# Optimization experiments

Measured on AMD Instinct MI355X. Metric: run time of the kernel, lower is better.

Reference implementation:

```python
import jax, jax.numpy as jnp
import numpy as np

NUM_HEADS = 8
HEAD_DIM = 32
ATTN_DIM = NUM_HEADS * HEAD_DIM  # 256
WINDOW_SIZES = (7, 5)
DILATIONS = (1, 2)
SCALE_FACTORS = (2, 4)


def conv1x1(x, W, b):
    # x: [B, C, H, W], W: [O, C], b: [O]
    return jnp.einsum('bchw,oc->bohw', x, W) + b[None, :, None, None]


def gather_neighbors(x, window, dilation):
    """Zero-padded dilated neighborhood gather.
    x: [B, C, h, w] -> neighbors [B, C, K, h, w], valid mask [K, h, w] (K = window**2)."""
    B, C, h, w = x.shape
    pad = dilation * (window // 2)
    xp = jnp.pad(x, ((0, 0), (0, 0), (pad, pad), (pad, pad)))
    mp = jnp.pad(jnp.ones((h, w), dtype=bool), ((pad, pad), (pad, pad)))
    neigh, masks = [], []
    for i in range(window):
        for j in range(window):
            dy, dx = dilation * i, dilation * j
            neigh.append(xp[:, :, dy:dy + h, dx:dx + w])
            masks.append(mp[dy:dy + h, dx:dx + w])
    return jnp.stack(neigh, axis=2), jnp.stack(masks, axis=0)


def align_to_query_grid(t, Hq, Wq, sf):
    """Repeat coarse-lattice candidates onto the fine query grid via anchor indexing."""
    y = jnp.minimum(jnp.arange(Hq) // sf, t.shape[-2] - 1)
    x = jnp.minimum(jnp.arange(Wq) // sf, t.shape[-1] - 1)
    return jnp.take(jnp.take(t, y, axis=-2), x, axis=-1)


def _forward(query, mems, Wq, bq, Wks, bks, Wvs, bvs, Wfuse, bfuse):
    B, _, Hq, Wq_ = query.shape
    q = conv1x1(query, Wq, bq)                                  # [B, attn, Hq, Wq]
    qh = q.reshape(B, NUM_HEADS, HEAD_DIM, Hq, Wq_)             # [B, n, d, H, W]
    scale = HEAD_DIM ** -0.5
    outs = []
    for s, mem in enumerate(mems):
        k = conv1x1(mem, Wks[s], bks[s])                        # [B, attn, hm, wm]
        v = conv1x1(mem, Wvs[s], bvs[s])
        kn, mask = gather_neighbors(k, WINDOW_SIZES[s], DILATIONS[s])  # [B, attn, K, hm, wm]
        vn, _ = gather_neighbors(v, WINDOW_SIZES[s], DILATIONS[s])
        K = kn.shape[2]
        hm, wm = kn.shape[-2:]
        kn = kn.reshape(B, NUM_HEADS, HEAD_DIM, K, hm, wm).transpose(0, 1, 3, 2, 4, 5)  # [B,n,K,d,hm,wm]
        vn = vn.reshape(B, NUM_HEADS, HEAD_DIM, K, hm, wm).transpose(0, 1, 3, 2, 4, 5)
        kn = align_to_query_grid(kn, Hq, Wq_, SCALE_FACTORS[s])  # [B,n,K,d,Hq,Wq]
        vn = align_to_query_grid(vn, Hq, Wq_, SCALE_FACTORS[s])
        mask_f = align_to_query_grid(mask, Hq, Wq_, SCALE_FACTORS[s])  # [K,Hq,Wq]
        scores = jnp.einsum('bndhw,bnkdhw->bnkhw', qh, kn) * scale
        neg = jnp.finfo(scores.dtype).min
        scores = jnp.where(mask_f[None, None], scores, neg)
        attn = jax.nn.softmax(scores, axis=2)                    # over K candidates
        o = jnp.einsum('bnkhw,bnkdhw->bndhw', attn, vn)
        outs.append(o.reshape(B, ATTN_DIM, Hq, Wq_))
    fused = jnp.concatenate(outs, axis=1)                        # [B, S*attn, Hq, Wq]
    return conv1x1(fused, Wfuse, bfuse)                          # [B, attn, Hq, Wq]


def setup_inputs() -> dict:
    key = jax.random.key(0)
    ks = jax.random.split(key, 16)
    std = 0.02
    inp = {
        'query': jax.random.normal(ks[0], (2, 256, 64, 64), jnp.float32),
        'mem0': jax.random.normal(ks[1], (2, 384, 32, 32), jnp.float32),
        'mem1': jax.random.normal(ks[2], (2, 768, 16, 16), jnp.float32),
        'Wq': jax.random.normal(ks[3], (ATTN_DIM, 256), jnp.float32) * std,
        'bq': jnp.zeros((ATTN_DIM,), jnp.float32),
        'Wk0': jax.random.normal(ks[4], (ATTN_DIM, 384), jnp.float32) * std,
        'bk0': jnp.zeros((ATTN_DIM,), jnp.float32),
        'Wv0': jax.random.normal(ks[5], (ATTN_DIM, 384), jnp.float32) * std,
        'bv0': jnp.zeros((ATTN_DIM,), jnp.float32),
        'Wk1': jax.random.normal(ks[6], (ATTN_DIM, 768), jnp.float32) * std,
        'bk1': jnp.zeros((ATTN_DIM,), jnp.float32),
        'Wv1': jax.random.normal(ks[7], (ATTN_DIM, 768), jnp.float32) * std,
        'bv1': jnp.zeros((ATTN_DIM,), jnp.float32),
        'Wfuse': jax.random.normal(ks[8], (ATTN_DIM, 2 * ATTN_DIM), jnp.float32) * std,
        'bfuse': jnp.zeros((ATTN_DIM,), jnp.float32),
    }
    return inp


def reference(query, mem0, mem1, Wq, bq, Wk0, bk0, Wv0, bv0, Wk1, bk1, Wv1, bv1, Wfuse, bfuse):
    return _forward(query, (mem0, mem1), Wq, bq, (Wk0, Wk1), (bk0, bk1), (Wv0, Wv1), (bv0, bv1), Wfuse, bfuse)
```

## Files before the change

### kernel.cpp

```cpp
#include <hip/hip_runtime.h>
#include <math.h>

typedef unsigned short u16;
typedef unsigned int u32;
typedef __attribute__((ext_vector_type(8))) short bf16x8;
typedef __attribute__((ext_vector_type(4))) float f32x4;

__device__ __forceinline__ u16 f2bf(float x) {
    u32 b = __builtin_bit_cast(u32, x);
    b += 0x7FFFu + ((b >> 16) & 1u);
    return (u16)(b >> 16);
}
__device__ __forceinline__ float bf2f(u16 u) {
    u32 b = ((u32)u) << 16;
    return __builtin_bit_cast(float, b);
}

__device__ __forceinline__ size_t sw_unit(int row, int c, int CC) {
    int slot = (c & 63) >> 3;
    return ((size_t)((row >> 7) * CC + (c >> 6)) << 10)
         + (size_t)((row & 127) << 3) + (size_t)(slot ^ (row & 7));
}

__device__ void prep_x(const float* __restrict__ X, int C, int HW, int bl, int PT,
                       u16* __restrict__ dh) {
    __shared__ float Xt[64][65];
    const int t = threadIdx.x;
    const int pt = bl % PT, ct = bl / PT;
    const int p0 = pt * 64, c0 = ct * 64;
    const int b = p0 / HW, hw0 = p0 % HW;
    #pragma unroll
    for (int i = 0; i < 16; i++) {
        int r = (t >> 6) + i * 4;
        Xt[r][t & 63] = X[(size_t)(b * C + c0 + r) * HW + hw0 + (t & 63)];
    }
    __syncthreads();
    const int CC = C >> 6;
    #pragma unroll
    for (int it = 0; it < 2; it++) {
        int id = t + it * 256;
        int px = id >> 3, sl = id & 7;
        bf16x8 hv;
        #pragma unroll
        for (int j = 0; j < 8; j++)
            hv[j] = (short)f2bf(Xt[sl * 8 + j][px]);
        size_t unit = sw_unit(p0 + px, c0 + sl * 8, CC);
        *(bf16x8*)(dh + unit * 8) = hv;
    }
}

__device__ void prep_w(const float* __restrict__ W, int C, int bl,
                       u16* __restrict__ dh) {
    const int t = threadIdx.x;
    const int ot = bl & 3, cc = bl >> 2;
    const int o0 = ot * 64, c0 = cc * 64;
    const int CC = C >> 6;
    #pragma unroll
    for (int it = 0; it < 2; it++) {
        int id = t + it * 256;
        int ol = id >> 3, sl = id & 7;
        int o = o0 + ol, c = c0 + sl * 8;
        const float* wp = W + (size_t)o * C + c;
        float4 a = *(const float4*)wp;
        float4 b2 = *(const float4*)(wp + 4);
        float xs[8] = {a.x, a.y, a.z, a.w, b2.x, b2.y, b2.z, b2.w};
        bf16x8 hv;
        #pragma unroll
        for (int j = 0; j < 8; j++)
            hv[j] = (short)f2bf(xs[j]);
        size_t unit = sw_unit(o, c, CC);
        *(bf16x8*)(dh + unit * 8) = hv;
    }
}

#define OFF_WQ 0
#define OFF_WK0 65536
#define OFF_WV0 163840
#define OFF_WK1 262144
#define OFF_WV1 458752
#define OFF_WFUSE 655360

__global__ __launch_bounds__(256) void prep_k(
    const float* __restrict__ query, const float* __restrict__ mem0, const float* __restrict__ mem1,
    const float* __restrict__ Wq, const float* __restrict__ Wk0, const float* __restrict__ Wv0,
    const float* __restrict__ Wk1, const float* __restrict__ Wv1, const float* __restrict__ Wfuse,
    u16* Xq_hi, u16* Xm0_hi, u16* Xm1_hi, u16* Whi)
{
    const int bx = blockIdx.x;
    if (bx < 512)      prep_x(query, 256, 4096, bx,       128, Xq_hi);
    else if (bx < 704) prep_x(mem0,  384, 1024, bx - 512,  32, Xm0_hi);
    else if (bx < 800) prep_x(mem1,  768,  256, bx - 704,   8, Xm1_hi);
    else {
        int r = bx - 800;
        if (r < 16)       prep_w(Wq,    256, r,       Whi + OFF_WQ);
        else if (r < 40)  prep_w(Wk0,   384, r - 16,  Whi + OFF_WK0);
        else if (r < 64)  prep_w(Wv0,   384, r - 40,  Whi + OFF_WV0);
        else if (r < 112) prep_w(Wk1,   768, r - 64,  Whi + OFF_WK1);
        else if (r < 160) prep_w(Wv1,   768, r - 112, Whi + OFF_WV1);
        else              prep_w(Wfuse, 512, r - 160, Whi + OFF_WFUSE);
    }
}

__device__ __forceinline__ void gemm_core(
    const u16* __restrict__ Ahi, const u16* __restrict__ Bhi,
    const float* __restrict__ bias, u16* __restrict__ Y,
    int CC, int am, int bn, u16* smem)
{
    const int t = threadIdx.x, lane = t & 63, w = t >> 6;
    const int l15 = lane & 15, kg = lane >> 4;

    f32x4 acc[2][4];
    #pragma unroll
    for (int a = 0; a < 2; a++)
        #pragma unroll
        for (int b2 = 0; b2 < 4; b2++)
            acc[a][b2] = (f32x4){0.f, 0.f, 0.f, 0.f};

    bf16x8 stgA[4], stgB[2];
    {
        const size_t aoff = ((size_t)(am * CC)) << 13;
        const size_t boff = ((((size_t)(bn >> 1) * CC) << 10) + (size_t)(bn & 1) * 512) * 8;
        #pragma unroll
        for (int it = 0; it < 4; it++)
            stgA[it] = *(const bf16x8*)(Ahi + aoff + (size_t)(t + it * 256) * 8);
        #pragma unroll
        for (int it = 0; it < 2; it++)
            stgB[it] = *(const bf16x8*)(Bhi + boff + (size_t)(t + it * 256) * 8);
    }

    for (int ck = 0; ck < CC; ck++) {
        __syncthreads();
        #pragma unroll
        for (int it = 0; it < 4; it++)
            *(bf16x8*)(smem + (size_t)(t + it * 256) * 8) = stgA[it];
        #pragma unroll
        for (int it = 0; it < 2; it++)
            *(bf16x8*)(smem + 8192 + (size_t)(t + it * 256) * 8) = stgB[it];
        __syncthreads();

        {
            const int cn = (ck + 1 < CC) ? ck + 1 : ck;
            const size_t aoff = ((size_t)(am * CC + cn)) << 13;
            const size_t boff = ((((size_t)(bn >> 1) * CC + cn) << 10) + (size_t)(bn & 1) * 512) * 8;
            #pragma unroll
            for (int it = 0; it < 4; it++)
                stgA[it] = *(const bf16x8*)(Ahi + aoff + (size_t)(t + it * 256) * 8);
            #pragma unroll
            for (int it = 0; it < 2; it++)
                stgB[it] = *(const bf16x8*)(Bhi + boff + (size_t)(t + it * 256) * 8);
        }

        #pragma unroll
        for (int kk = 0; kk < 2; kk++) {
            bf16x8 ah[2], bh[4];
            #pragma unroll
            for (int tr = 0; tr < 2; tr++) {
                int row = w * 32 + tr * 16 + l15;
                int off = row * 64 + (((kk * 4 + kg) ^ (row & 7)) << 3);
                ah[tr] = *(const bf16x8*)(smem + off);
            }
            #pragma unroll
            for (int tc = 0; tc < 4; tc++) {
                int row = tc * 16 + l15;
                int off = row * 64 + (((kk * 4 + kg) ^ (row & 7)) << 3);
                bh[tc] = *(const bf16x8*)(smem + 8192 + off);
            }
            #pragma unroll
            for (int tr = 0; tr < 2; tr++)
                #pragma unroll
                for (int tc = 0; tc < 4; tc++)
                    acc[tr][tc] = __builtin_amdgcn_mfma_f32_16x16x32_bf16(ah[tr], bh[tc], acc[tr][tc], 0, 0, 0);
        }
    }

    float bv[4];
    #pragma unroll
    for (int tc = 0; tc < 4; tc++)
        bv[tc] = bias[bn * 64 + tc * 16 + l15];
    #pragma unroll
    for (int tr = 0; tr < 2; tr++) {
        #pragma unroll
        for (int i = 0; i < 4; i++) {
            int rp = am * 128 + w * 32 + tr * 16 + kg * 4 + i;
            u16* yr = Y + (size_t)rp * 256 + bn * 64 + l15;
            #pragma unroll
            for (int tc = 0; tc < 4; tc++)
                yr[tc * 16] = f2bf(acc[tr][tc][i] + bv[tc]);
        }
    }
}

__global__ __launch_bounds__(256) void projmm_k(
    const u16* __restrict__ Xq_hi, const u16* __restrict__ Xm0_hi,
    const u16* __restrict__ Xm1_hi, const u16* __restrict__ Whi,
    const float* __restrict__ bq, const float* __restrict__ bk0, const float* __restrict__ bv0,
    const float* __restrict__ bk1, const float* __restrict__ bv1,
    u16* qT, u16* k0T, u16* v0T, u16* k1T, u16* v1T)
{
    __shared__ u16 smem[12288];
    const int bx = blockIdx.x;
    if (bx < 256) {
        gemm_core(Xq_hi, Whi + OFF_WQ, bq, qT, 4, bx >> 2, bx & 3, smem);
    } else if (bx < 320) {
        const int r = bx - 256;
        gemm_core(Xm0_hi, Whi + OFF_WK0, bk0, k0T, 6, r >> 2, r & 3, smem);
    } else if (bx < 384) {
        const int r = bx - 320;
        gemm_core(Xm0_hi, Whi + OFF_WV0, bv0, v0T, 6, r >> 2, r & 3, smem);
    } else if (bx < 400) {
        const int r = bx - 384;
        gemm_core(Xm1_hi, Whi + OFF_WK1, bk1, k1T, 12, r >> 2, r & 3, smem);
    } else {
        const int r = bx - 400;
        gemm_core(Xm1_hi, Whi + OFF_WV1, bv1, v1T, 12, r >> 2, r & 3, smem);
    }
}

__global__ __launch_bounds__(256) void fusemm_k(
    const u16* __restrict__ Whi, const u16* __restrict__ fhi,
    const float* __restrict__ bias, float* __restrict__ out)
{
    __shared__ u16 smem[12288];
    const int t = threadIdx.x, lane = t & 63, w = t >> 6;
    const int wr = w >> 1, wc = w & 1;
    const int l15 = lane & 15;
    const int am = blockIdx.x & 3, bn = blockIdx.x >> 2;
    const u16* A = Whi + OFF_WFUSE;

    f32x4 acc[2][4];
    #pragma unroll
    for (int a = 0; a < 2; a++)
        #pragma unroll
        for (int b2 = 0; b2 < 4; b2++)
            acc[a][b2] = (f32x4){0.f, 0.f, 0.f, 0.f};

    bf16x8 stgA[2], stgB[4];
    {
        const size_t aoff = (((size_t)(am >> 1) * 8) << 10) + (size_t)(am & 1) * 512;
        const size_t boff = ((size_t)(bn * 8)) << 10;
        #pragma unroll
        for (int it = 0; it < 2; it++)
            stgA[it] = *(const bf16x8*)(A + (aoff + t + it * 256) * 8);
        #pragma unroll
        for (int it = 0; it < 4; it++)
            stgB[it] = *(const bf16x8*)(fhi + (boff + t + it * 256) * 8);
    }

    for (int ck = 0; ck < 8; ck++) {
        __syncthreads();
        #pragma unroll
        for (int it = 0; it < 2; it++)
            *(bf16x8*)(smem + (size_t)(t + it * 256) * 8) = stgA[it];
        #pragma unroll
        for (int it = 0; it < 4; it++)
            *(bf16x8*)(smem + 4096 + (size_t)(t + it * 256) * 8) = stgB[it];
        __syncthreads();

        {
            const int cn = (ck + 1 < 8) ? ck + 1 : ck;
            const size_t aoff = (((size_t)(am >> 1) * 8 + cn) << 10) + (size_t)(am & 1) * 512;
            const size_t boff = ((size_t)(bn * 8 + cn)) << 10;
            #pragma unroll
            for (int it = 0; it < 2; it++)
                stgA[it] = *(const bf16x8*)(A + (aoff + t + it * 256) * 8);
            #pragma unroll
            for (int it = 0; it < 4; it++)
                stgB[it] = *(const bf16x8*)(fhi + (boff + t + it * 256) * 8);
        }

        #pragma unroll
        for (int kk = 0; kk < 2; kk++) {
            bf16x8 ah[2], bh[4];
            #pragma unroll
            for (int tr = 0; tr < 2; tr++) {
                int row = wr * 32 + tr * 16 + l15;
                int off = row * 64 + (((kk * 4 + (lane >> 4)) ^ (row & 7)) << 3);
                ah[tr] = *(const bf16x8*)(smem + off);
            }
            #pragma unroll
            for (int tc = 0; tc < 4; tc++) {
                int row = wc * 64 + tc * 16 + l15;
                int off = row * 64 + (((kk * 4 + (lane >> 4)) ^ (row & 7)) << 3);
                bh[tc] = *(const bf16x8*)(smem + 4096 + off);
            }
            #pragma unroll
            for (int tr = 0; tr < 2; tr++)
                #pragma unroll
                for (int tc = 0; tc < 4; tc++)
                    acc[tr][tc] = __builtin_amdgcn_mfma_f32_16x16x32_bf16(ah[tr], bh[tc], acc[tr][tc], 0, 0, 0);
        }
    }

    #pragma unroll
    for (int tr = 0; tr < 2; tr++) {
        #pragma unroll
        for (int i = 0; i < 4; i++) {
            const int o = am * 64 + wr * 32 + tr * 16 + ((lane >> 4) << 2) + i;
            const float bv = bias[o];
            #pragma unroll
            for (int tc = 0; tc < 4; tc++) {
                const int pcol = bn * 128 + wc * 64 + tc * 16 + l15;
                out[(size_t)((pcol >> 12) * 256 + o) * 4096 + (pcol & 4095)] = acc[tr][tc][i] + bv;
            }
        }
    }
}

template<int SCALE>
__device__ __forceinline__ void attn_mfma(
    const u16* __restrict__ qT, const u16* __restrict__ kT,
    const u16* __restrict__ vT, u16* __restrict__ fhi,
    int b, int n, int ty, int tx, int lane, u16* s_lds)
{
    constexpr int HM = SCALE ? 16 : 32;
    constexpr int NT = SCALE ? 2 : 4;
    const int qy0 = ty * 4, qx0 = tx * 4;
    const int ay0 = SCALE ? (qy0 >> 2) : (qy0 >> 1);
    const int ax0 = SCALE ? (qx0 >> 2) : (qx0 >> 1);
    const int l15 = lane & 15, kg = lane >> 4;

    const int pA = (b * 64 + qy0 + (l15 >> 2)) * 64 + qx0 + (l15 & 3);
    const bf16x8 qf = *(const bf16x8*)(qT + (size_t)pA * 256 + n * 32 + kg * 8);

    f32x4 s[NT];
    #pragma unroll
    for (int t = 0; t < NT; t++) {
        const int cand = t * 16 + l15;
        const int wy = SCALE ? (cand / 6) : (cand >> 3);
        const int wx = SCALE ? (cand % 6) : (cand & 7);
        const int my = SCALE ? (ay0 + (wy - 2) * 2) : (ay0 - 3 + wy);
        const int mx = SCALE ? (ax0 + (wx - 2) * 2) : (ax0 - 3 + wx);
        const int myc = min(max(my, 0), HM - 1), mxc = min(max(mx, 0), HM - 1);
        const bf16x8 kf = *(const bf16x8*)(kT + (size_t)((b * HM + myc) * HM + mxc) * 256 + n * 32 + kg * 8);
        s[t] = __builtin_amdgcn_mfma_f32_16x16x32_bf16(qf, kf, (f32x4){0.f, 0.f, 0.f, 0.f}, 0, 0, 0);
    }

    const float scl = 0.17677669529663687f;
    float sv[NT][4];
    #pragma unroll
    for (int t = 0; t < NT; t++) {
        const int cand = t * 16 + l15;
        const int wy = SCALE ? (cand / 6) : (cand >> 3);
        const int wx = SCALE ? (cand % 6) : (cand & 7);
        const int my = SCALE ? (ay0 + (wy - 2) * 2) : (ay0 - 3 + wy);
        const int mx = SCALE ? (ax0 + (wx - 2) * 2) : (ax0 - 3 + wx);
        const bool inb = (my >= 0) && (my < HM) && (mx >= 0) && (mx < HM);
        #pragma unroll
        for (int i = 0; i < 4; i++) {
            bool ok;
            if (SCALE) {
                ok = inb && (wy < 5) && (wx < 5);
            } else {
                const int r = kg * 4 + i;
                const int dy2 = (r >> 2) >> 1, dx2 = (r & 3) >> 1;
                ok = inb && ((u32)(wy - dy2) <= 6u) && ((u32)(wx - dx2) <= 6u);
            }
            sv[t][i] = ok ? s[t][i] * scl : -1e30f;
        }
    }

    float linv[4];
    #pragma unroll
    for (int i = 0; i < 4; i++) {
        float m = sv[0][i];
        #pragma unroll
        for (int t = 1; t < NT; t++) m = fmaxf(m, sv[t][i]);
        #pragma unroll
        for (int dd = 1; dd < 16; dd <<= 1) m = fmaxf(m, __shfl_xor(m, dd, 64));
        float l = 0.f;
        #pragma unroll
        for (int t = 0; t < NT; t++) { sv[t][i] = __expf(sv[t][i] - m); l += sv[t][i]; }
        #pragma unroll
        for (int dd = 1; dd < 16; dd <<= 1) l += __shfl_xor(l, dd, 64);
        linv[i] = 1.f / l;
    }

    #pragma unroll
    for (int t = 0; t < NT; t++)
        #pragma unroll
        for (int i = 0; i < 4; i++)
            s_lds[(kg * 4 + i) * 68 + t * 16 + l15] = f2bf(sv[t][i]);

    f32x4 o[2] = {(f32x4){0.f,0.f,0.f,0.f}, (f32x4){0.f,0.f,0.f,0.f}};
    #pragma unroll
    for (int h = 0; h < NT / 2; h++) {
        const bf16x8 pa = *(const bf16x8*)(s_lds + l15 * 68 + h * 32 + kg * 8);
        #pragma unroll
        for (int c = 0; c < 2; c++) {
            bf16x8 vf;
            #pragma unroll
            for (int j = 0; j < 8; j++) {
                const int cand = h * 32 + kg * 8 + j;
                const int wy = SCALE ? (cand / 6) : (cand >> 3);
                const int wx = SCALE ? (cand % 6) : (cand & 7);
                int my = SCALE ? (ay0 + (wy - 2) * 2) : (ay0 - 3 + wy);
                int mx = SCALE ? (ax0 + (wx - 2) * 2) : (ax0 - 3 + wx);
                my = min(max(my, 0), HM - 1); mx = min(max(mx, 0), HM - 1);
                vf[j] = (short)vT[(size_t)((b * HM + my) * HM + mx) * 256 + n * 32 + c * 16 + l15];
            }
            o[c] = __builtin_amdgcn_mfma_f32_16x16x32_bf16(pa, vf, o[c], 0, 0, 0);
        }
    }

    #pragma unroll
    for (int c = 0; c < 2; c++) {
        #pragma unroll
        for (int i = 0; i < 4; i++) {
            const int r = kg * 4 + i;
            const int p = (b * 64 + qy0 + (r >> 2)) * 64 + qx0 + (r & 3);
            const int ch = (SCALE ? 256 : 0) + n * 32 + c * 16 + l15;
            fhi[sw_unit(p, ch, 8) * 8 + (ch & 7)] = f2bf(o[c][i] * linv[i]);
        }
    }
}

__global__ __launch_bounds__(256) void attn_k(
    const u16* __restrict__ qT,
    const u16* __restrict__ k0T, const u16* __restrict__ v0T,
    const u16* __restrict__ k1T, const u16* __restrict__ v1T,
    u16* __restrict__ fhi)
{
    __shared__ u16 s_lds[4][16 * 68];
    const int t = threadIdx.x, w = t >> 6, lane = t & 63;
    const int bx = blockIdx.x;
    const int sc = bx >> 10;
    const int tile = (bx & 1023) * 4 + w;
    const int b = tile >> 11, n = (tile >> 8) & 7;
    const int ty = (tile >> 4) & 15, tx = tile & 15;
    if (sc == 0) attn_mfma<0>(qT, k0T, v0T, fhi, b, n, ty, tx, lane, s_lds[w]);
    else         attn_mfma<1>(qT, k1T, v1T, fhi, b, n, ty, tx, lane, s_lds[w]);
}

extern "C" void kernel_launch(void* const* d_in, const int* in_sizes, int n_in,
                              void* d_out, int out_size, void* d_ws, size_t ws_size,
                              hipStream_t stream)
{
    const float* query = (const float*)d_in[0];
    const float* mem0  = (const float*)d_in[1];
    const float* mem1  = (const float*)d_in[2];
    const float* Wq    = (const float*)d_in[3];  const float* bq    = (const float*)d_in[4];
    const float* Wk0   = (const float*)d_in[5];  const float* bk0   = (const float*)d_in[6];
    const float* Wv0   = (const float*)d_in[7];  const float* bv0   = (const float*)d_in[8];
    const float* Wk1   = (const float*)d_in[9];  const float* bk1   = (const float*)d_in[10];
    const float* Wv1   = (const float*)d_in[11]; const float* bv1   = (const float*)d_in[12];
    const float* Wfuse = (const float*)d_in[13]; const float* bfuse = (const float*)d_in[14];
    float* out = (float*)d_out;

    char* ws = (char*)d_ws;
    u16* qT       = (u16*)(ws + 0);
    u16* k0T      = (u16*)(ws + 8388608);
    u16* v0T      = (u16*)(ws + 10485760);
    u16* k1T      = (u16*)(ws + 12582912);
    u16* v1T      = (u16*)(ws + 13107200);
    u16* Whi      = (u16*)(ws + 13631488);
    u16* Xm0_hi   = (u16*)(ws + 16777216);
    u16* Xm1_hi   = (u16*)(ws + 19922944);
    u16* Xq_hi    = (u16*)(ws + 21495808);
    u16* fhi      = Xq_hi;

    prep_k<<<dim3(992), 256, 0, stream>>>(
        query, mem0, mem1, Wq, Wk0, Wv0, Wk1, Wv1, Wfuse,
        Xq_hi, Xm0_hi, Xm1_hi, Whi);

    projmm_k<<<dim3(416), 256, 0, stream>>>(
        Xq_hi, Xm0_hi, Xm1_hi, Whi,
        bq, bk0, bv0, bk1, bv1, qT, k0T, v0T, k1T, v1T);

    attn_k<<<dim3(2048), 256, 0, stream>>>(qT, k0T, v0T, k1T, v1T, fhi);

    fusemm_k<<<dim3(256), 256, 0, stream>>>(Whi, fhi, bfuse, out);
}
```

Measured before the change: 45.71 us.

## Stage shared K/V halo tile in LDS for 2x2 query tiles per block

Each block now covers an 8x8 query region (four 4x4 wave tiles) for one head. It cooperatively loads a 10x10 clamped halo of K and V head slices into shared memory, and the waves then gather keys and values from LDS instead of making scattered global loads. This cuts redundant global and L2 traffic for overlapping neighborhoods. The cost is an added __syncthreads, about 12.8KB more LDS per block, and some halo cells loaded but never used.

```diff
diff --git a/kernel.cpp b/kernel.cpp
--- a/kernel.cpp
+++ b/kernel.cpp
@@ -307,16 +307,16 @@
 }
 
 template<int SCALE>
-__device__ __forceinline__ void attn_mfma(
-    const u16* __restrict__ qT, const u16* __restrict__ kT,
-    const u16* __restrict__ vT, u16* __restrict__ fhi,
-    int b, int n, int ty, int tx, int lane, u16* s_lds)
+__device__ __forceinline__ void attn_core(
+    const u16* __restrict__ qT, const u16* __restrict__ sK,
+    const u16* __restrict__ sV, u16* __restrict__ fhi,
+    int b, int n, int gy, int gx, int sy, int sx, int lane, u16* s_lds)
 {
     constexpr int HM = SCALE ? 16 : 32;
     constexpr int NT = SCALE ? 2 : 4;
-    const int qy0 = ty * 4, qx0 = tx * 4;
-    const int ay0 = SCALE ? (qy0 >> 2) : (qy0 >> 1);
-    const int ax0 = SCALE ? (qx0 >> 2) : (qx0 >> 1);
+    const int qy0 = gy * 8 + sy * 4, qx0 = gx * 8 + sx * 4;
+    const int ay0 = SCALE ? (gy * 2 + sy) : (gy * 4 + sy * 2);
+    const int ax0 = SCALE ? (gx * 2 + sx) : (gx * 4 + sx * 2);
     const int l15 = lane & 15, kg = lane >> 4;
 
     const int pA = (b * 64 + qy0 + (l15 >> 2)) * 64 + qx0 + (l15 & 3);
@@ -328,10 +328,9 @@
         const int cand = t * 16 + l15;
         const int wy = SCALE ? (cand / 6) : (cand >> 3);
         const int wx = SCALE ? (cand % 6) : (cand & 7);
-        const int my = SCALE ? (ay0 + (wy - 2) * 2) : (ay0 - 3 + wy);
-        const int mx = SCALE ? (ax0 + (wx - 2) * 2) : (ax0 - 3 + wx);
-        const int myc = min(max(my, 0), HM - 1), mxc = min(max(mx, 0), HM - 1);
-        const bf16x8 kf = *(const bf16x8*)(kT + (size_t)((b * HM + myc) * HM + mxc) * 256 + n * 32 + kg * 8);
+        const int fy = min(SCALE ? (sy + (wy - 2) * 2 + 4) : (sy * 2 + wy), 9);
+        const int fx = min(SCALE ? (sx + (wx - 2) * 2 + 4) : (sx * 2 + wx), 9);
+        const bf16x8 kf = *(const bf16x8*)(sK + (fy * 10 + fx) * 32 + kg * 8);
         s[t] = __builtin_amdgcn_mfma_f32_16x16x32_bf16(qf, kf, (f32x4){0.f, 0.f, 0.f, 0.f}, 0, 0, 0);
     }
 
@@ -393,10 +392,9 @@
                 const int cand = h * 32 + kg * 8 + j;
                 const int wy = SCALE ? (cand / 6) : (cand >> 3);
                 const int wx = SCALE ? (cand % 6) : (cand & 7);
-                int my = SCALE ? (ay0 + (wy - 2) * 2) : (ay0 - 3 + wy);
-                int mx = SCALE ? (ax0 + (wx - 2) * 2) : (ax0 - 3 + wx);
-                my = min(max(my, 0), HM - 1); mx = min(max(mx, 0), HM - 1);
-                vf[j] = (short)vT[(size_t)((b * HM + my) * HM + mx) * 256 + n * 32 + c * 16 + l15];
+                const int fy = min(SCALE ? (sy + (wy - 2) * 2 + 4) : (sy * 2 + wy), 9);
+                const int fx = min(SCALE ? (sx + (wx - 2) * 2 + 4) : (sx * 2 + wx), 9);
+                vf[j] = (short)sV[(fy * 10 + fx) * 32 + c * 16 + l15];
             }
             o[c] = __builtin_amdgcn_mfma_f32_16x16x32_bf16(pa, vf, o[c], 0, 0, 0);
         }
@@ -420,15 +418,41 @@
     const u16* __restrict__ k1T, const u16* __restrict__ v1T,
     u16* __restrict__ fhi)
 {
+    __shared__ u16 sK[3200];
+    __shared__ u16 sV[3200];
     __shared__ u16 s_lds[4][16 * 68];
     const int t = threadIdx.x, w = t >> 6, lane = t & 63;
     const int bx = blockIdx.x;
     const int sc = bx >> 10;
-    const int tile = (bx & 1023) * 4 + w;
-    const int b = tile >> 11, n = (tile >> 8) & 7;
-    const int ty = (tile >> 4) & 15, tx = tile & 15;
-    if (sc == 0) attn_mfma<0>(qT, k0T, v0T, fhi, b, n, ty, tx, lane, s_lds[w]);
-    else         attn_mfma<1>(qT, k1T, v1T, fhi, b, n, ty, tx, lane, s_lds[w]);
+    const int r = bx & 1023;
+    const int b = r >> 9, n = (r >> 6) & 7;
+    const int gy = (r >> 3) & 7, gx = r & 7;
+
+    {
+        const u16* kT = sc ? k1T : k0T;
+        const u16* vT = sc ? v1T : v0T;
+        const int HM  = sc ? 16 : 32;
+        const int my0 = sc ? (gy * 2 - 4) : (gy * 4 - 3);
+        const int mx0 = sc ? (gx * 2 - 4) : (gx * 4 - 3);
+        #pragma unroll
+        for (int p = 0; p < 2; p++) {
+            const int idx = t + p * 256;
+            if (idx < 400) {
+                const int px = idx >> 2, seg = idx & 3;
+                const int fy = px / 10, fx = px % 10;
+                const int ry = min(max(my0 + fy, 0), HM - 1);
+                const int rx = min(max(mx0 + fx, 0), HM - 1);
+                const size_t src = (size_t)((b * HM + ry) * HM + rx) * 256 + n * 32 + seg * 8;
+                *(bf16x8*)(sK + px * 32 + seg * 8) = *(const bf16x8*)(kT + src);
+                *(bf16x8*)(sV + px * 32 + seg * 8) = *(const bf16x8*)(vT + src);
+            }
+        }
+    }
+    __syncthreads();
+
+    const int sy = w >> 1, sx = w & 1;
+    if (sc == 0) attn_core<0>(qT, sK, sV, fhi, b, n, gy, gx, sy, sx, lane, s_lds[w]);
+    else         attn_core<1>(qT, sK, sV, fhi, b, n, gy, gx, sy, sx, lane, s_lds[w]);
 }
 
 extern "C" void kernel_launch(void* const* d_in, const int* in_sizes, int n_in,
```

Measured after the change: 46.42 us. No clear change (+1.5%).
